# Kernel optimization log

Hardware: AMD Instinct MI355X
Metric: run time of the kernel (lower is better)

The kernel has to match this reference:

```python
import jax, jax.numpy as jnp
import numpy as np

B, C_IN, H, W = 16, 128, 224, 224
C_OUT, KH, KW = 256, 3, 3
STRIDE = (2, 3)
PAD = 1


def setup_inputs() -> dict:
    key = jax.random.key(0)
    kx, kw, kb = jax.random.split(key, 3)
    x = jax.random.normal(kx, (B, C_IN, H, W), dtype=jnp.float32)
    weight = jax.random.normal(kw, (C_OUT, C_IN, KH, KW), dtype=jnp.float32)
    bias = jax.random.normal(kb, (C_OUT,), dtype=jnp.float32)
    return {"x": x, "weight": weight, "bias": bias}


def reference(x, weight, bias):
    # Faithful conv2d: zero-pad by 1 on each side, stride (2,3), kernel 3x3,
    # per-output-channel dot product + bias (same math as the quadruple-loop torch code).
    out = jax.lax.conv_general_dilated(
        x, weight,
        window_strides=STRIDE,
        padding=[(PAD, PAD), (PAD, PAD)],
        dimension_numbers=("NCHW", "OIHW", "NCHW"),
    )
    return out + bias[None, :, None, None]
```

## Files before the change

### kernel.cpp

```cpp
#include <hip/hip_runtime.h>
#include <cstdint>

constexpr int B_   = 16;
constexpr int CIN  = 128;
constexpr int H_   = 224;
constexpr int W_   = 224;
constexpr int COUT = 256;
constexpr int HOUT = 112;
constexpr int WOUT = 75;

constexpr int CI_SC = 16;
constexpr int KSC_R = 144;
constexpr int KP    = 160;
constexpr int NSC   = 8;
constexpr int THREADS = 256;

constexpr int WS_SH8  = COUT * KP * NSC / 8;
constexpr size_t WS_NEED = (size_t)WS_SH8 * 16;

typedef float  f32x4   __attribute__((ext_vector_type(4)));
typedef short  short8  __attribute__((ext_vector_type(8)));

struct U64x2 { unsigned long long lo, hi; };
__device__ inline short8 bc8(unsigned long long a, unsigned long long b) {
  U64x2 u{a, b};
  return __builtin_bit_cast(short8, u);
}

__device__ inline unsigned cvtpk(float a, float b) {
  unsigned r;
  asm("v_cvt_pk_bf16_f32 %0, %1, %2" : "=v"(r) : "v"(a), "v"(b));
  return r;
}

__global__ __launch_bounds__(256) void wprep(const float* __restrict__ wgt,
                                             uint4* __restrict__ ws) {
  int o  = blockIdx.x * 256 + threadIdx.x;
  int co = o & 255;
  int t  = o >> 8;
  int g  = t & 3;
  int u  = t >> 2;
  int kc = u % 5;
  int sc = u / 5;
  int kloc = kc * 32 + g * 8;
  float f[8];
  if (kloc < KSC_R) {
    const float* p = wgt + (size_t)co * 1152 + sc * KSC_R + kloc;
    float4 a = *(const float4*)p;
    float4 b = *(const float4*)(p + 4);
    f[0] = a.x; f[1] = a.y; f[2] = a.z; f[3] = a.w;
    f[4] = b.x; f[5] = b.y; f[6] = b.z; f[7] = b.w;
  } else {
#pragma unroll
    for (int e = 0; e < 8; ++e) f[e] = 0.f;
  }
  ws[o] = uint4{cvtpk(f[0], f[1]), cvtpk(f[2], f[3]), cvtpk(f[4], f[5]), cvtpk(f[6], f[7])};
}

__device__ __forceinline__ short8 load_bq(const float* q, int kc, int g) {
  if (kc == 4 && g >= 2) return short8{};
  const float* s = q + kc * 32;
  float4 x0 = *(const float4*)s, x1 = *(const float4*)(s + 4);
  uint4 u{cvtpk(x0.x, x0.y), cvtpk(x0.z, x0.w), cvtpk(x1.x, x1.y), cvtpk(x1.z, x1.w)};
  return __builtin_bit_cast(short8, u);
}

#define TR_ISSUE(S, KC)                                                                   \
  {                                                                                       \
    unsigned a_ = abase + (unsigned)((KC) * 5120);                                        \
    asm volatile("ds_read_b64_tr_b16 %0, %1"             : "=v"(S##0) : "v"(a_));         \
    asm volatile("ds_read_b64_tr_b16 %0, %1 offset:640"  : "=v"(S##1) : "v"(a_));         \
    asm volatile("ds_read_b64_tr_b16 %0, %1 offset:128"  : "=v"(S##2) : "v"(a_));         \
    asm volatile("ds_read_b64_tr_b16 %0, %1 offset:768"  : "=v"(S##3) : "v"(a_));         \
    asm volatile("ds_read_b64_tr_b16 %0, %1 offset:256"  : "=v"(S##4) : "v"(a_));         \
    asm volatile("ds_read_b64_tr_b16 %0, %1 offset:896"  : "=v"(S##5) : "v"(a_));         \
    asm volatile("ds_read_b64_tr_b16 %0, %1 offset:384"  : "=v"(S##6) : "v"(a_));         \
    asm volatile("ds_read_b64_tr_b16 %0, %1 offset:1024" : "=v"(S##7) : "v"(a_));         \
    asm volatile("ds_read_b64_tr_b16 %0, %1 offset:512"  : "=v"(S##8) : "v"(a_));         \
    asm volatile("ds_read_b64_tr_b16 %0, %1 offset:1152" : "=v"(S##9) : "v"(a_));         \
  }

#define BLOADR(X, KC)                                                                     \
  X##0 = wsb[(KC) * 1024];                                                                \
  X##1 = wsb[(KC) * 1024 + 16];                                                           \
  X##2 = wsb[(KC) * 1024 + 32];                                                           \
  X##3 = wsb[(KC) * 1024 + 48];

#define WAITLG(N)                                                                         \
  asm volatile("s_waitcnt lgkmcnt(" #N ")" ::: "memory");                                 \
  __builtin_amdgcn_sched_barrier(0);

#define MFMA_SET(S, B0, B1, B2, B3)                                                       \
  {                                                                                       \
    short8 a0_ = bc8(S##0, S##1);                                                         \
    short8 a1_ = bc8(S##2, S##3);                                                         \
    short8 a2_ = bc8(S##4, S##5);                                                         \
    short8 a3_ = bc8(S##6, S##7);                                                         \
    short8 a4_ = bc8(S##8, S##9);                                                         \
    __builtin_amdgcn_s_setprio(1);                                                        \
    acc[0][0] = __builtin_amdgcn_mfma_f32_16x16x32_bf16(a0_, B0, acc[0][0], 0, 0, 0);     \
    acc[0][1] = __builtin_amdgcn_mfma_f32_16x16x32_bf16(a0_, B1, acc[0][1], 0, 0, 0);     \
    acc[0][2] = __builtin_amdgcn_mfma_f32_16x16x32_bf16(a0_, B2, acc[0][2], 0, 0, 0);     \
    acc[0][3] = __builtin_amdgcn_mfma_f32_16x16x32_bf16(a0_, B3, acc[0][3], 0, 0, 0);     \
    acc[1][0] = __builtin_amdgcn_mfma_f32_16x16x32_bf16(a1_, B0, acc[1][0], 0, 0, 0);     \
    acc[1][1] = __builtin_amdgcn_mfma_f32_16x16x32_bf16(a1_, B1, acc[1][1], 0, 0, 0);     \
    acc[1][2] = __builtin_amdgcn_mfma_f32_16x16x32_bf16(a1_, B2, acc[1][2], 0, 0, 0);     \
    acc[1][3] = __builtin_amdgcn_mfma_f32_16x16x32_bf16(a1_, B3, acc[1][3], 0, 0, 0);     \
    acc[2][0] = __builtin_amdgcn_mfma_f32_16x16x32_bf16(a2_, B0, acc[2][0], 0, 0, 0);     \
    acc[2][1] = __builtin_amdgcn_mfma_f32_16x16x32_bf16(a2_, B1, acc[2][1], 0, 0, 0);     \
    acc[2][2] = __builtin_amdgcn_mfma_f32_16x16x32_bf16(a2_, B2, acc[2][2], 0, 0, 0);     \
    acc[2][3] = __builtin_amdgcn_mfma_f32_16x16x32_bf16(a2_, B3, acc[2][3], 0, 0, 0);     \
    acc[3][0] = __builtin_amdgcn_mfma_f32_16x16x32_bf16(a3_, B0, acc[3][0], 0, 0, 0);     \
    acc[3][1] = __builtin_amdgcn_mfma_f32_16x16x32_bf16(a3_, B1, acc[3][1], 0, 0, 0);     \
    acc[3][2] = __builtin_amdgcn_mfma_f32_16x16x32_bf16(a3_, B2, acc[3][2], 0, 0, 0);     \
    acc[3][3] = __builtin_amdgcn_mfma_f32_16x16x32_bf16(a3_, B3, acc[3][3], 0, 0, 0);     \
    acc[4][0] = __builtin_amdgcn_mfma_f32_16x16x32_bf16(a4_, B0, acc[4][0], 0, 0, 0);     \
    acc[4][1] = __builtin_amdgcn_mfma_f32_16x16x32_bf16(a4_, B1, acc[4][1], 0, 0, 0);     \
    acc[4][2] = __builtin_amdgcn_mfma_f32_16x16x32_bf16(a4_, B2, acc[4][2], 0, 0, 0);     \
    acc[4][3] = __builtin_amdgcn_mfma_f32_16x16x32_bf16(a4_, B3, acc[4][3], 0, 0, 0);     \
    __builtin_amdgcn_s_setprio(0);                                                        \
  }

#define STAGE_LOAD(SC)                                                                    \
  {                                                                                       \
    const float* xs_ = xb + (size_t)((SC) & 7) * (CI_SC * H_ * W_);                       \
    _Pragma("unroll")                                                                     \
    for (int j = 0; j < 3; ++j) {                                                         \
      int it  = tid + THREADS * j;                                                        \
      int gg  = it % 19;                                                                  \
      int rid = it / 19;                                                                  \
      int ci  = rid & 15;                                                                 \
      int kh  = rid >> 4;                                                                 \
      int ih  = 2 * oh - 1 + kh;                                                          \
      bool rowok = (unsigned)ih < (unsigned)H_;                                           \
      int ro  = (ci * H_ + (rowok ? ih : 0)) * W_;                                        \
      int iwb = 12 * gg;                                                                  \
      const float* ap = xs_ + (ro + iwb);                                                 \
      pa[j] = *(const float4*)ap;                                                         \
      pb[j] = *(const float4*)(ap + 4);                                                   \
      pc[j] = *(const float4*)(xs_ + (ro + (iwb + 8 > 220 ? 220 : iwb + 8)));             \
      pm[j] = xs_[ro + iwb - (gg ? 1 : 0)];                                               \
    }                                                                                     \
  }

template <int WS>
__global__ __launch_bounds__(THREADS, 2) void conv_mfma(
    const float* __restrict__ x, const float* __restrict__ wgt,
    const short8* __restrict__ wbf, const float* __restrict__ bias,
    float* __restrict__ out) {

  __shared__ __align__(16) unsigned char smem[KP * 80 * 2];

  int Lid = (blockIdx.x & 7) * 224 + (blockIdx.x >> 3);
  int oh  = Lid % 112;
  int b   = Lid / 112;

  const int tid   = threadIdx.x;
  const int lane  = tid & 63;
  const int cogrp = tid >> 6;
  const int g     = lane >> 4;
  const int l15   = lane & 15;

  const float* xb = x + (size_t)b * CIN * H_ * W_;
  const int coB_  = cogrp * 64 + l15;

  const unsigned sbase = (unsigned)(uintptr_t)&smem[0];
  const unsigned abase = sbase + (unsigned)(g * 1280 + l15 * 8);

  if (tid < 160) {
    *reinterpret_cast<uint4*>(&smem[23040 + tid * 16]) = uint4{0u, 0u, 0u, 0u};
  }

  f32x4 acc[5][4];
#pragma unroll
  for (int mf = 0; mf < 5; ++mf)
#pragma unroll
    for (int cf = 0; cf < 4; ++cf)
#pragma unroll
      for (int i = 0; i < 4; ++i) acc[mf][cf][i] = 0.f;

  unsigned long long tA0, tA1, tA2, tA3, tA4, tA5, tA6, tA7, tA8, tA9;
  unsigned long long tB0, tB1, tB2, tB3, tB4, tB5, tB6, tB7, tB8, tB9;
  short8 bX0, bX1, bX2, bX3, bY0, bY1, bY2, bY3, bZ0, bZ1, bZ2, bZ3;
  float4 pa[3], pb[3], pc[3];
  float  pm[3];

  STAGE_LOAD(0);

  for (int sc = 0; sc < NSC; ++sc) {
    const short8* wsb = wbf + (size_t)sc * 5120 + g * 256 + cogrp * 64 + l15;

    if (WS) { BLOADR(bX, 0) BLOADR(bY, 1) }

    if (sc) __syncthreads();

    const float* xs = xb + (size_t)sc * (CI_SC * H_ * W_);
#pragma unroll
    for (int j = 0; j < 4; ++j) {
      int it = tid + THREADS * j;
      if (j < 3 || it < 912) {
        int gg  = it % 19;
        int rid = it / 19;
        int ci  = rid & 15;
        int kh  = rid >> 4;
        int ih  = 2 * oh - 1 + kh;
        bool rowok = (unsigned)ih < (unsigned)H_;
        unsigned mAj = rowok ? 0xFFFFFFFFu : 0u;
        unsigned mFj = mAj & (gg ? 0xFFFFFFFFu : 0xFFFF0000u);

        float4 a4, b4, c4;
        float fm1;
        if (j < 3) {
          a4 = pa[j]; b4 = pb[j]; c4 = pc[j]; fm1 = pm[j];
        } else {
          int ro  = (ci * H_ + (rowok ? ih : 0)) * W_;
          int iwb = 12 * gg;
          const float* ap = xs + (ro + iwb);
          a4 = *(const float4*)ap;
          b4 = *(const float4*)(ap + 4);
          c4 = *(const float4*)(xs + (ro + (iwb + 8 > 220 ? 220 : iwb + 8)));
          fm1 = xs[ro + iwb - (gg ? 1 : 0)];
        }

        int k = ci * 9 + kh * 3;
        int m = 4 * gg;
        unsigned base = (unsigned)(((k >> 2) * 5 + (m >> 4)) * 128 + (m & 15) * 2);
        unsigned o0 = base + (unsigned)((k & 3) * 32);
        unsigned o1 = base + (unsigned)(((k + 1) & 3) * 32) + (((k + 1) >> 2) - (k >> 2)) * 640u;
        unsigned o2 = base + (unsigned)(((k + 2) & 3) * 32) + (((k + 2) >> 2) - (k >> 2)) * 640u;

        unsigned l0 = cvtpk(fm1,  a4.z) & mFj;
        unsigned h0 = cvtpk(b4.y, c4.x) & mAj;
        unsigned l1 = cvtpk(a4.x, a4.w) & mAj;
        unsigned h1 = cvtpk(b4.z, c4.y) & mAj;
        unsigned l2 = cvtpk(a4.y, b4.x) & mAj;
        unsigned h2 = cvtpk(b4.w, c4.z) & mAj;
        *(uint2*)&smem[o0] = make_uint2(l0, h0);
        *(uint2*)&smem[o1] = make_uint2(l1, h1);
        *(uint2*)&smem[o2] = make_uint2(l2, h2);
      }
    }
    __syncthreads();

    if (WS) {
      TR_ISSUE(tA, 0);
      TR_ISSUE(tB, 1);
      BLOADR(bZ, 2)
      WAITLG(10);
      MFMA_SET(tA, bX0, bX1, bX2, bX3);
      TR_ISSUE(tA, 2);
      BLOADR(bX, 3)
      WAITLG(10);
      MFMA_SET(tB, bY0, bY1, bY2, bY3);
      STAGE_LOAD(sc + 1);
      TR_ISSUE(tB, 3);
      BLOADR(bY, 4)
      WAITLG(10);
      MFMA_SET(tA, bZ0, bZ1, bZ2, bZ3);
      TR_ISSUE(tA, 4);
      WAITLG(10);
      MFMA_SET(tB, bX0, bX1, bX2, bX3);
      WAITLG(0);
      MFMA_SET(tA, bY0, bY1, bY2, bY3);
    } else {
      const float* q0 = wgt + (size_t)coB_ * 1152 + sc * 144 + g * 8;
      const float* q1 = q0 + (size_t)16 * 1152;
      const float* q2 = q0 + (size_t)32 * 1152;
      const float* q3 = q0 + (size_t)48 * 1152;
      STAGE_LOAD(sc + 1);
#pragma unroll
      for (int kc = 0; kc < 5; ++kc) {
        short8 c0 = load_bq(q0, kc, g), c1 = load_bq(q1, kc, g);
        short8 c2 = load_bq(q2, kc, g), c3 = load_bq(q3, kc, g);
        TR_ISSUE(tA, kc);
        WAITLG(0);
        MFMA_SET(tA, c0, c1, c2, c3);
      }
    }
  }

  float bv0 = bias[coB_];
  float bv1 = bias[coB_ + 16];
  float bv2 = bias[coB_ + 32];
  float bv3 = bias[coB_ + 48];
  size_t ob0 = (((size_t)b * COUT + coB_) * HOUT + oh) * WOUT;
  size_t ob1 = ob0 + (size_t)16 * HOUT * WOUT;
  size_t ob2 = ob0 + (size_t)32 * HOUT * WOUT;
  size_t ob3 = ob0 + (size_t)48 * HOUT * WOUT;
#pragma unroll
  for (int mf = 0; mf < 5; ++mf) {
    int owb = mf * 16 + g * 4;
#pragma unroll
    for (int r = 0; r < 4; ++r) {
      int ow = owb + r;
      if (ow < WOUT) {
        out[ob0 + ow] = acc[mf][0][r] + bv0;
        out[ob1 + ow] = acc[mf][1][r] + bv1;
        out[ob2 + ow] = acc[mf][2][r] + bv2;
        out[ob3 + ow] = acc[mf][3][r] + bv3;
      }
    }
  }
}

extern "C" void kernel_launch(void* const* d_in, const int* in_sizes, int n_in,
                              void* d_out, int out_size, void* d_ws, size_t ws_size,
                              hipStream_t stream) {
  const float* x    = (const float*)d_in[0];
  const float* wgt  = (const float*)d_in[1];
  const float* bias = (const float*)d_in[2];
  float* out        = (float*)d_out;

  dim3 grid(16 * 112);
  dim3 block(THREADS);

  if (ws_size >= WS_NEED) {
    wprep<<<dim3(WS_SH8 / 256), dim3(256), 0, stream>>>(wgt, (uint4*)d_ws);
    conv_mfma<1><<<grid, block, 0, stream>>>(x, wgt, (const short8*)d_ws, bias, out);
  } else {
    conv_mfma<0><<<grid, block, 0, stream>>>(x, wgt, (const short8*)d_ws, bias, out);
  }
}
```

Baseline: 222.9 us.

## Double-buffer LDS input tiles so staging overlaps MFMA compute

Splits the LDS input tile into two buffers. The next channel slice is converted and written into the idle buffer while MFMAs read the current one, and the global prefetch now runs two stages ahead. This removes one barrier per iteration and the serialized write phase before compute. In exchange, LDS use doubles to about 50 KB per block, which may limit occupancy at two blocks per CU, and register pressure rises from interleaving the write code inside the MFMA schedule.

Result: slower. 322.6 us (+44.7%).

```diff
diff --git a/kernel.cpp b/kernel.cpp
--- a/kernel.cpp
+++ b/kernel.cpp
@@ -17,6 +17,9 @@
 
 constexpr int WS_SH8  = COUT * KP * NSC / 8;
 constexpr size_t WS_NEED = (size_t)WS_SH8 * 16;
+
+constexpr int ABUF  = 25600;
+constexpr int LDS_TOT = 2 * ABUF;
 
 typedef float  f32x4   __attribute__((ext_vector_type(4)));
 typedef short  short8  __attribute__((ext_vector_type(8)));
@@ -65,9 +68,9 @@
   return __builtin_bit_cast(short8, u);
 }
 
-#define TR_ISSUE(S, KC)                                                                   \
+#define TR_ISSUE(S, KC, BUFO)                                                             \
   {                                                                                       \
-    unsigned a_ = abase + (unsigned)((KC) * 5120);                                        \
+    unsigned a_ = abase + (BUFO) + (unsigned)((KC) * 5120);                               \
     asm volatile("ds_read_b64_tr_b16 %0, %1"             : "=v"(S##0) : "v"(a_));         \
     asm volatile("ds_read_b64_tr_b16 %0, %1 offset:640"  : "=v"(S##1) : "v"(a_));         \
     asm volatile("ds_read_b64_tr_b16 %0, %1 offset:128"  : "=v"(S##2) : "v"(a_));         \
@@ -80,11 +83,11 @@
     asm volatile("ds_read_b64_tr_b16 %0, %1 offset:1152" : "=v"(S##9) : "v"(a_));         \
   }
 
-#define BLOADR(X, KC)                                                                     \
-  X##0 = wsb[(KC) * 1024];                                                                \
-  X##1 = wsb[(KC) * 1024 + 16];                                                           \
-  X##2 = wsb[(KC) * 1024 + 32];                                                           \
-  X##3 = wsb[(KC) * 1024 + 48];
+#define BLOADR(X, P, KC)                                                                  \
+  X##0 = (P)[(KC) * 1024];                                                                \
+  X##1 = (P)[(KC) * 1024 + 16];                                                           \
+  X##2 = (P)[(KC) * 1024 + 32];                                                           \
+  X##3 = (P)[(KC) * 1024 + 48];
 
 #define WAITLG(N)                                                                         \
   asm volatile("s_waitcnt lgkmcnt(" #N ")" ::: "memory");                                 \
@@ -143,13 +146,60 @@
     }                                                                                     \
   }
 
+#define STAGE_WRITE(SCW, BUFO)                                                            \
+  {                                                                                       \
+    const float* xsw = xb + (size_t)((SCW) & 7) * (CI_SC * H_ * W_);                      \
+    _Pragma("unroll")                                                                     \
+    for (int j = 0; j < 4; ++j) {                                                         \
+      int it = tid + THREADS * j;                                                         \
+      if (j < 3 || it < 912) {                                                            \
+        int gg  = it % 19;                                                                \
+        int rid = it / 19;                                                                \
+        int ci  = rid & 15;                                                               \
+        int kh  = rid >> 4;                                                               \
+        int ih  = 2 * oh - 1 + kh;                                                        \
+        bool rowok = (unsigned)ih < (unsigned)H_;                                         \
+        unsigned mAj = rowok ? 0xFFFFFFFFu : 0u;                                          \
+        unsigned mFj = mAj & (gg ? 0xFFFFFFFFu : 0xFFFF0000u);                            \
+        float4 a4, b4, c4;                                                                \
+        float fm1;                                                                        \
+        if (j < 3) {                                                                      \
+          a4 = pa[j]; b4 = pb[j]; c4 = pc[j]; fm1 = pm[j];                                \
+        } else {                                                                          \
+          int ro  = (ci * H_ + (rowok ? ih : 0)) * W_;                                    \
+          int iwb = 12 * gg;                                                              \
+          const float* ap = xsw + (ro + iwb);                                             \
+          a4 = *(const float4*)ap;                                                        \
+          b4 = *(const float4*)(ap + 4);                                                  \
+          c4 = *(const float4*)(xsw + (ro + (iwb + 8 > 220 ? 220 : iwb + 8)));            \
+          fm1 = xsw[ro + iwb - (gg ? 1 : 0)];                                             \
+        }                                                                                 \
+        int k = ci * 9 + kh * 3;                                                          \
+        int m = 4 * gg;                                                                   \
+        unsigned base = (unsigned)(((k >> 2) * 5 + (m >> 4)) * 128 + (m & 15) * 2) + (BUFO); \
+        unsigned o0 = base + (unsigned)((k & 3) * 32);                                    \
+        unsigned o1 = base + (unsigned)(((k + 1) & 3) * 32) + (((k + 1) >> 2) - (k >> 2)) * 640u; \
+        unsigned o2 = base + (unsigned)(((k + 2) & 3) * 32) + (((k + 2) >> 2) - (k >> 2)) * 640u; \
+        unsigned l0 = cvtpk(fm1,  a4.z) & mFj;                                            \
+        unsigned h0 = cvtpk(b4.y, c4.x) & mAj;                                            \
+        unsigned l1 = cvtpk(a4.x, a4.w) & mAj;                                            \
+        unsigned h1 = cvtpk(b4.z, c4.y) & mAj;                                            \
+        unsigned l2 = cvtpk(a4.y, b4.x) & mAj;                                            \
+        unsigned h2 = cvtpk(b4.w, c4.z) & mAj;                                            \
+        *(uint2*)&smem[o0] = make_uint2(l0, h0);                                          \
+        *(uint2*)&smem[o1] = make_uint2(l1, h1);                                          \
+        *(uint2*)&smem[o2] = make_uint2(l2, h2);                                          \
+      }                                                                                   \
+    }                                                                                     \
+  }
+
 template <int WS>
 __global__ __launch_bounds__(THREADS, 2) void conv_mfma(
     const float* __restrict__ x, const float* __restrict__ wgt,
     const short8* __restrict__ wbf, const float* __restrict__ bias,
     float* __restrict__ out) {
 
-  __shared__ __align__(16) unsigned char smem[KP * 80 * 2];
+  __shared__ __align__(16) unsigned char smem[LDS_TOT];
 
   int Lid = (blockIdx.x & 7) * 224 + (blockIdx.x >> 3);
   int oh  = Lid % 112;
@@ -168,7 +218,8 @@
   const unsigned abase = sbase + (unsigned)(g * 1280 + l15 * 8);
 
   if (tid < 160) {
-    *reinterpret_cast<uint4*>(&smem[23040 + tid * 16]) = uint4{0u, 0u, 0u, 0u};
+    *reinterpret_cast<uint4*>(&smem[23040 + tid * 16])        = uint4{0u, 0u, 0u, 0u};
+    *reinterpret_cast<uint4*>(&smem[ABUF + 23040 + tid * 16]) = uint4{0u, 0u, 0u, 0u};
   }
 
   f32x4 acc[5][4];
@@ -186,97 +237,71 @@
   float  pm[3];
 
   STAGE_LOAD(0);
+  STAGE_WRITE(0, 0u);
+  if (WS) {
+    const short8* w0 = wbf + g * 256 + cogrp * 64 + l15;
+    BLOADR(bX, w0, 0)
+    BLOADR(bY, w0, 1)
+  }
+  __syncthreads();
+  STAGE_LOAD(1);
 
   for (int sc = 0; sc < NSC; ++sc) {
-    const short8* wsb = wbf + (size_t)sc * 5120 + g * 256 + cogrp * 64 + l15;
-
-    if (WS) { BLOADR(bX, 0) BLOADR(bY, 1) }
-
-    if (sc) __syncthreads();
-
-    const float* xs = xb + (size_t)sc * (CI_SC * H_ * W_);
-#pragma unroll
-    for (int j = 0; j < 4; ++j) {
-      int it = tid + THREADS * j;
-      if (j < 3 || it < 912) {
-        int gg  = it % 19;
-        int rid = it / 19;
-        int ci  = rid & 15;
-        int kh  = rid >> 4;
-        int ih  = 2 * oh - 1 + kh;
-        bool rowok = (unsigned)ih < (unsigned)H_;
-        unsigned mAj = rowok ? 0xFFFFFFFFu : 0u;
-        unsigned mFj = mAj & (gg ? 0xFFFFFFFFu : 0xFFFF0000u);
-
-        float4 a4, b4, c4;
-        float fm1;
-        if (j < 3) {
-          a4 = pa[j]; b4 = pb[j]; c4 = pc[j]; fm1 = pm[j];
-        } else {
-          int ro  = (ci * H_ + (rowok ? ih : 0)) * W_;
-          int iwb = 12 * gg;
-          const float* ap = xs + (ro + iwb);
-          a4 = *(const float4*)ap;
-          b4 = *(const float4*)(ap + 4);
-          c4 = *(const float4*)(xs + (ro + (iwb + 8 > 220 ? 220 : iwb + 8)));
-          fm1 = xs[ro + iwb - (gg ? 1 : 0)];
-        }
-
-        int k = ci * 9 + kh * 3;
-        int m = 4 * gg;
-        unsigned base = (unsigned)(((k >> 2) * 5 + (m >> 4)) * 128 + (m & 15) * 2);
-        unsigned o0 = base + (unsigned)((k & 3) * 32);
-        unsigned o1 = base + (unsigned)(((k + 1) & 3) * 32) + (((k + 1) >> 2) - (k >> 2)) * 640u;
-        unsigned o2 = base + (unsigned)(((k + 2) & 3) * 32) + (((k + 2) >> 2) - (k >> 2)) * 640u;
-
-        unsigned l0 = cvtpk(fm1,  a4.z) & mFj;
-        unsigned h0 = cvtpk(b4.y, c4.x) & mAj;
-        unsigned l1 = cvtpk(a4.x, a4.w) & mAj;
-        unsigned h1 = cvtpk(b4.z, c4.y) & mAj;
-        unsigned l2 = cvtpk(a4.y, b4.x) & mAj;
-        unsigned h2 = cvtpk(b4.w, c4.z) & mAj;
-        *(uint2*)&smem[o0] = make_uint2(l0, h0);
-        *(uint2*)&smem[o1] = make_uint2(l1, h1);
-        *(uint2*)&smem[o2] = make_uint2(l2, h2);
-      }
-    }
-    __syncthreads();
+    const unsigned bufo  = (unsigned)((sc & 1) * ABUF);
+    const unsigned nbufo = bufo ^ (unsigned)ABUF;
 
     if (WS) {
-      TR_ISSUE(tA, 0);
-      TR_ISSUE(tB, 1);
-      BLOADR(bZ, 2)
+      const short8* wsb  = wbf + (size_t)sc * 5120 + g * 256 + cogrp * 64 + l15;
+      const short8* wsbn = wbf + (size_t)((sc + 1) & 7) * 5120 + g * 256 + cogrp * 64 + l15;
+
+      TR_ISSUE(tA, 0, bufo);
+      TR_ISSUE(tB, 1, bufo);
+      BLOADR(bZ, wsb, 2)
       WAITLG(10);
       MFMA_SET(tA, bX0, bX1, bX2, bX3);
-      TR_ISSUE(tA, 2);
-      BLOADR(bX, 3)
+      TR_ISSUE(tA, 2, bufo);
+      BLOADR(bX, wsb, 3)
       WAITLG(10);
       MFMA_SET(tB, bY0, bY1, bY2, bY3);
-      STAGE_LOAD(sc + 1);
-      TR_ISSUE(tB, 3);
-      BLOADR(bY, 4)
+      if (sc < 7) {
+        STAGE_WRITE(sc + 1, nbufo);
+      }
+      if (sc < 6) {
+        STAGE_LOAD(sc + 2);
+      }
+      TR_ISSUE(tB, 3, bufo);
+      BLOADR(bY, wsb, 4)
       WAITLG(10);
       MFMA_SET(tA, bZ0, bZ1, bZ2, bZ3);
-      TR_ISSUE(tA, 4);
+      TR_ISSUE(tA, 4, bufo);
       WAITLG(10);
       MFMA_SET(tB, bX0, bX1, bX2, bX3);
+      BLOADR(bX, wsbn, 0)
       WAITLG(0);
       MFMA_SET(tA, bY0, bY1, bY2, bY3);
+      BLOADR(bY, wsbn, 1)
     } else {
       const float* q0 = wgt + (size_t)coB_ * 1152 + sc * 144 + g * 8;
       const float* q1 = q0 + (size_t)16 * 1152;
       const float* q2 = q0 + (size_t)32 * 1152;
       const float* q3 = q0 + (size_t)48 * 1152;
-      STAGE_LOAD(sc + 1);
+      if (sc < 7) {
+        STAGE_WRITE(sc + 1, nbufo);
+      }
+      if (sc < 6) {
+        STAGE_LOAD(sc + 2);
+      }
 #pragma unroll
       for (int kc = 0; kc < 5; ++kc) {
         short8 c0 = load_bq(q0, kc, g), c1 = load_bq(q1, kc, g);
         short8 c2 = load_bq(q2, kc, g), c3 = load_bq(q3, kc, g);
-        TR_ISSUE(tA, kc);
+        TR_ISSUE(tA, kc, bufo);
         WAITLG(0);
         MFMA_SET(tA, c0, c1, c2, c3);
       }
     }
+
+    __syncthreads();
   }
 
   float bv0 = bias[coB_];
```
